# Performance work log

Hardware: AMD Instinct MI355X
Metric: run time of the kernel (lower is better)

## Reference

```python
import jax, jax.numpy as jnp
import numpy as np


def _pred_clampedgrad(x):
    # causal neighbors with zero padding (NCHW)
    n = jnp.pad(x[:, :, :-1, :], ((0, 0), (0, 0), (1, 0), (0, 0)))
    w = jnp.pad(x[:, :, :, :-1], ((0, 0), (0, 0), (0, 0), (1, 0)))
    nw = jnp.pad(x[:, :, :-1, :-1], ((0, 0), (0, 0), (1, 0), (1, 0)))
    pred = jnp.clip(n + w - nw, jnp.minimum(n, w), jnp.maximum(n, w))
    return x - pred


def _calc_entropy_differentiable(x, nbits):
    # Equivalent to the original O(nlevels*N) loop: relu(1-|x-sym|) is exactly
    # linear interpolation onto the two neighboring integer bins, so we build
    # the per-(b,c) soft histogram with one O(N) scatter-add.
    nlevels = 1 << nbits
    xs = (x + 1.0) * ((nlevels - 1) / 2.0)  # map [-1,1] -> [0, nlevels-1]
    B, C, H, W = xs.shape
    flat = xs.reshape(B * C, H * W)
    f = jnp.floor(flat)
    frac = flat - f
    i0 = f.astype(jnp.int32)
    bc = jnp.arange(B * C)[:, None]
    hist = jnp.zeros((B * C, nlevels), xs.dtype)
    hist = hist.at[bc, i0].add(1.0 - frac, mode='drop')  # OOB bins contribute 0 (relu clamp)
    hist = hist.at[bc, i0 + 1].add(frac, mode='drop')
    prob = hist / (H * W)
    safe = jnp.where(prob > 0, prob, 1.0)  # nan_to_num(-0*log2(0)) -> 0
    term = -prob * jnp.log2(safe)
    entropy = jnp.sum(term, axis=1)  # [B*C]
    return jnp.mean(entropy) / nbits


def setup_inputs() -> dict:
    key = jax.random.key(0)
    x = jax.random.uniform(key, (32, 3, 512, 512), jnp.float32, -1.0, 1.0)
    params = jnp.array([-1.0, 0.0, 0.5, 0.0, 0.0, -1.0,
                        0.0, 0.0, 0.0, 0.5, 0.0, 0.0], jnp.float32)
    return {"x": x, "params": params}


def reference(x, params):
    p = params
    r0, g0, b0 = x[:, 0:1], x[:, 1:2], x[:, 2:3]
    r1 = r0 + (p[0] * g0 + p[1] * b0)
    g1 = g0 + (p[2] * r1 + p[3] * b0)
    b1 = b0 + (p[4] * r1 + p[5] * g1)
    r2 = r1 + (p[6] * g1 + p[7] * b1)
    g2 = g1 + (p[8] * r2 + p[9] * b1)
    b2 = b1 + (p[10] * r2 + p[11] * g2)
    y = jnp.concatenate((r2, g2, b2), axis=1)
    y = jnp.fmod(y + 1.0, 2.0) - 1.0  # fmod keeps sign of dividend, same as torch.fmod
    res = _pred_clampedgrad(y)
    return _calc_entropy_differentiable(res, 8)
```

## Files before the change

### kernel.cpp

```cpp
#include <hip/hip_runtime.h>

#define IMG_H 512
#define IMG_W 512
#define RPB 8
#define NROW (RPB + 1)
#define NLEV 256
#define NB 32
#define NC 3
#define NYB (IMG_H / RPB)
#define BINS (NC * NLEV)
#define NBLK (NB * NYB)
#define NTHR 256
#define NWAVE (NTHR / 64)

__device__ uint2    g_pk[NBLK * BINS];
__device__ unsigned g_dropQ[NBLK * NC];
__device__ float    g_ent[NB * NC];
__device__ unsigned g_done = 0;

__device__ __forceinline__ float wrap1(float v) {
    float a = v + 1.0f;
    return a - 2.0f * truncf(0.5f * a) - 1.0f;
}

__device__ __forceinline__ void xform(float& r, float& g, float& bl,
                                      const float* __restrict__ p) {
    float r1 = r + (p[0] * g + p[1] * bl);
    float g1 = g + (p[2] * r1 + p[3] * bl);
    float b1 = bl + (p[4] * r1 + p[5] * g1);
    float r2 = r1 + (p[6] * g1 + p[7] * b1);
    float g2 = g1 + (p[8] * r2 + p[9] * b1);
    float b2 = b1 + (p[10] * r2 + p[11] * g2);
    r = wrap1(r2); g = wrap1(g2); bl = wrap1(b2);
}

__device__ __forceinline__ void accum(float y, float n, float w, float nw,
                                      unsigned* __restrict__ h,
                                      unsigned* __restrict__ drop) {
    float lo = fminf(n, w), hi = fmaxf(n, w);
    float pred = fminf(fmaxf(n + w - nw, lo), hi);
    float xs = (y - pred + 1.0f) * 127.5f;
    float f = floorf(xs);
    float frac = xs - f;
    int i0 = (int)f;
    unsigned fq = (unsigned)(frac * 1024.0f + 0.5f);
    int j0 = (i0 < 0) ? i0 + NLEV : i0;
    if ((unsigned)j0 < (unsigned)NLEV) {
        atomicAdd(&h[j0], (1u << 21) | fq);
        if (i0 == NLEV - 1) atomicAdd(drop, fq);
    }
}

__global__ __launch_bounds__(NTHR) void hist_kernel(const float* __restrict__ x,
                                                    const float* __restrict__ params) {
    __shared__ unsigned lhw[NWAVE][NC][NLEV];
    __shared__ float bnd[NWAVE][NROW][NC];
    __shared__ unsigned dropw[NC];
    const int tid = threadIdx.x;
    const int b = blockIdx.x;
    const int yb = blockIdx.y;
    const int r0 = yb * RPB;
    const int wv = tid >> 6;
    const int lane = tid & 63;

    unsigned* lp = &lhw[0][0][0];
#pragma unroll
    for (int i = tid; i < NWAVE * BINS; i += NTHR) lp[i] = 0u;
    if (tid < NC) dropw[tid] = 0u;

    float p[12];
#pragma unroll
    for (int i = 0; i < 12; ++i) p[i] = params[i];

    const int hw = IMG_H * IMG_W;
    const float2* base = (const float2*)(x + (size_t)(b * 3) * hw) + tid;

    float a0[NROW], a1[NROW], c0[NROW], c1[NROW], e0[NROW], e1[NROW];
#pragma unroll
    for (int rr = 0; rr < NROW; ++rr) {
        if (rr > 0 || r0 > 0) {
            int ro = (r0 - 1 + rr) * (IMG_W / 2);
            float2 vr = base[ro];
            float2 vg = base[ro + hw / 2];
            float2 vb = base[ro + hw];
            a0[rr] = vr.x; a1[rr] = vr.y;
            c0[rr] = vg.x; c1[rr] = vg.y;
            e0[rr] = vb.x; e1[rr] = vb.y;
        } else {
            a0[rr] = a1[rr] = c0[rr] = c1[rr] = e0[rr] = e1[rr] = 0.0f;
        }
    }

#pragma unroll
    for (int rr = 0; rr < NROW; ++rr) {
        xform(a0[rr], c0[rr], e0[rr], p);
        xform(a1[rr], c1[rr], e1[rr], p);
    }

    if (lane == 63) {
#pragma unroll
        for (int rr = 0; rr < NROW; ++rr) {
            bnd[wv][rr][0] = a1[rr];
            bnd[wv][rr][1] = c1[rr];
            bnd[wv][rr][2] = e1[rr];
        }
    }
    __syncthreads();

    const int pw = (wv > 0) ? wv - 1 : 0;
    const float* pwb = &bnd[pw][0][0];
    float bv = pwb[lane < NROW * NC ? lane : 0];
    const bool lz = (lane == 0);

#define RDL(rr, ch) __int_as_float(__builtin_amdgcn_readlane(__float_as_int(bv), (rr) * NC + (ch)))

    unsigned* h0 = &lhw[wv][0][0];
    unsigned* h1 = &lhw[wv][1][0];
    unsigned* h2 = &lhw[wv][2][0];

    float nA0 = a0[0], nA1 = a1[0];
    float nC0 = c0[0], nC1 = c1[0];
    float nE0 = e0[0], nE1 = e1[0];
    float nwA = __shfl_up(a1[0], 1);
    float nwC = __shfl_up(c1[0], 1);
    float nwE = __shfl_up(e1[0], 1);
    {
        float bA = (wv > 0) ? RDL(0, 0) : 0.0f;
        float bC = (wv > 0) ? RDL(0, 1) : 0.0f;
        float bE = (wv > 0) ? RDL(0, 2) : 0.0f;
        if (lz) { nwA = bA; nwC = bC; nwE = bE; }
    }

#pragma unroll
    for (int rr = 1; rr < NROW; ++rr) {
        float uA0 = a0[rr], uA1 = a1[rr];
        float uC0 = c0[rr], uC1 = c1[rr];
        float uE0 = e0[rr], uE1 = e1[rr];
        float vA = __shfl_up(uA1, 1);
        float vC = __shfl_up(uC1, 1);
        float vE = __shfl_up(uE1, 1);
        float bA = (wv > 0) ? RDL(rr, 0) : 0.0f;
        float bC = (wv > 0) ? RDL(rr, 1) : 0.0f;
        float bE = (wv > 0) ? RDL(rr, 2) : 0.0f;
        if (lz) { vA = bA; vC = bC; vE = bE; }
        accum(uA0, nA0, vA, nwA, h0, &dropw[0]);
        accum(uA1, nA1, uA0, nA0, h0, &dropw[0]);
        accum(uC0, nC0, vC, nwC, h1, &dropw[1]);
        accum(uC1, nC1, uC0, nC0, h1, &dropw[1]);
        accum(uE0, nE0, vE, nwE, h2, &dropw[2]);
        accum(uE1, nE1, uE0, nE0, h2, &dropw[2]);
        nwA = vA; nA0 = uA0; nA1 = uA1;
        nwC = vC; nC0 = uC0; nC1 = uC1;
        nwE = vE; nE0 = uE0; nE1 = uE1;
    }
    __syncthreads();

    const int blk = b * NYB + yb;
    uint2* dp = g_pk + (size_t)blk * BINS;
#pragma unroll
    for (int i = tid; i < BINS; i += NTHR) {
        int c = i >> 8, bin = i & 255;
        unsigned cs = 0, qs = 0;
#pragma unroll
        for (int w2 = 0; w2 < NWAVE; ++w2) {
            unsigned v = lhw[w2][c][bin];
            cs += v >> 21;
            qs += v & 0x1FFFFFu;
        }
        dp[i] = make_uint2(cs, qs);
    }
    if (tid < NC) g_dropQ[blk * NC + tid] = dropw[tid];
}

__global__ __launch_bounds__(256) void ent_kernel(float* __restrict__ out) {
    const int g = blockIdx.x;
    const int b = g / NC, c = g % NC;
    const int t = threadIdx.x;
    const uint2* sp = g_pk + (size_t)b * NYB * BINS + c * NLEV + t;
    unsigned cnt = 0, fq = 0;
#pragma unroll
    for (int y = 0; y < NYB; ++y) {
        uint2 v = sp[(size_t)y * BINS];
        cnt += v.x;
        fq  += v.y;
    }
    __shared__ unsigned fsb[NLEV];
    __shared__ unsigned dsh;
    fsb[t] = fq;
    if (t < 64) {
        unsigned d = g_dropQ[(b * NYB + t) * NC + c];
#pragma unroll
        for (int o = 32; o > 0; o >>= 1) d += __shfl_down(d, o);
        if (t == 0) dsh = d;
    }
    __syncthreads();
    unsigned passq = (t == 0) ? (fsb[NLEV - 1] - dsh) : fsb[t - 1];
    float hist = (float)cnt + ((float)passq - (float)fq) * (1.0f / 1024.0f);
    float pr = hist * (1.0f / (float)(IMG_H * IMG_W));
    float term = (pr > 0.0f) ? -pr * log2f(pr) : 0.0f;
#pragma unroll
    for (int o = 32; o > 0; o >>= 1) term += __shfl_down(term, o);
    __shared__ float red[4];
    if ((t & 63) == 0) red[t >> 6] = term;
    __syncthreads();
    if (t == 0) {
        g_ent[g] = red[0] + red[1] + red[2] + red[3];
        __threadfence();
        unsigned prev = atomicAdd(&g_done, 1u);
        if (prev == NB * NC - 1) {
            __threadfence();
            float s = 0.0f;
            for (int i = 0; i < NB * NC; ++i) s += g_ent[i];
            out[0] = s * (1.0f / (float)(NB * NC) / 8.0f);
            g_done = 0;
        }
    }
}

extern "C" void kernel_launch(void* const* d_in, const int* in_sizes, int n_in,
                              void* d_out, int out_size, void* d_ws, size_t ws_size,
                              hipStream_t stream) {
    const float* x = (const float*)d_in[0];
    const float* params = (const float*)d_in[1];
    float* out = (float*)d_out;

    dim3 grid(NB, NYB);
    hist_kernel<<<grid, NTHR, 0, stream>>>(x, params);
    ent_kernel<<<NB * NC, 256, 0, stream>>>(out);
}
```

Measured before the change: 44.76 us.

## Accumulate per-image histograms with global 64-bit atomics and register drop sums

Each histogram block now adds its packed count/fraction bins straight into a per-(batch,channel) 64-bit global accumulator with atomics, replacing the per-block partial histogram buffer. The entropy kernel reads a single value per bin and zeroes it for the next call, so it no longer reduces 64 partials. Drop counts for the top bin are summed in registers, reduced across the wave with shuffles, and committed with one shared atomic per wave instead of a shared atomic per hit. The cost is contention on global atomics (64 blocks per image hit the same 768 bins), plus a reliance on the accumulators starting at zero on the first launch.

```diff
diff --git a/kernel.cpp b/kernel.cpp
--- a/kernel.cpp
+++ b/kernel.cpp
@@ -13,8 +13,8 @@
 #define NTHR 256
 #define NWAVE (NTHR / 64)
 
-__device__ uint2    g_pk[NBLK * BINS];
-__device__ unsigned g_dropQ[NBLK * NC];
+__device__ unsigned long long g_acc[NB * NC * NLEV];
+__device__ unsigned g_dropA[NB * NC];
 __device__ float    g_ent[NB * NC];
 __device__ unsigned g_done = 0;
 
@@ -36,7 +36,7 @@
 
 __device__ __forceinline__ void accum(float y, float n, float w, float nw,
                                       unsigned* __restrict__ h,
-                                      unsigned* __restrict__ drop) {
+                                      unsigned& drop) {
     float lo = fminf(n, w), hi = fmaxf(n, w);
     float pred = fminf(fmaxf(n + w - nw, lo), hi);
     float xs = (y - pred + 1.0f) * 127.5f;
@@ -47,8 +47,8 @@
     int j0 = (i0 < 0) ? i0 + NLEV : i0;
     if ((unsigned)j0 < (unsigned)NLEV) {
         atomicAdd(&h[j0], (1u << 21) | fq);
-        if (i0 == NLEV - 1) atomicAdd(drop, fq);
-    }
+    }
+    drop += (i0 == NLEV - 1) ? fq : 0u;
 }
 
 __global__ __launch_bounds__(NTHR) void hist_kernel(const float* __restrict__ x,
@@ -117,6 +117,7 @@
     unsigned* h0 = &lhw[wv][0][0];
     unsigned* h1 = &lhw[wv][1][0];
     unsigned* h2 = &lhw[wv][2][0];
+    unsigned dr0 = 0u, dr1 = 0u, dr2 = 0u;
 
     float nA0 = a0[0], nA1 = a1[0];
     float nC0 = c0[0], nC1 = c1[0];
@@ -143,20 +144,31 @@
         float bC = (wv > 0) ? RDL(rr, 1) : 0.0f;
         float bE = (wv > 0) ? RDL(rr, 2) : 0.0f;
         if (lz) { vA = bA; vC = bC; vE = bE; }
-        accum(uA0, nA0, vA, nwA, h0, &dropw[0]);
-        accum(uA1, nA1, uA0, nA0, h0, &dropw[0]);
-        accum(uC0, nC0, vC, nwC, h1, &dropw[1]);
-        accum(uC1, nC1, uC0, nC0, h1, &dropw[1]);
-        accum(uE0, nE0, vE, nwE, h2, &dropw[2]);
-        accum(uE1, nE1, uE0, nE0, h2, &dropw[2]);
+        accum(uA0, nA0, vA, nwA, h0, dr0);
+        accum(uA1, nA1, uA0, nA0, h0, dr0);
+        accum(uC0, nC0, vC, nwC, h1, dr1);
+        accum(uC1, nC1, uC0, nC0, h1, dr1);
+        accum(uE0, nE0, vE, nwE, h2, dr2);
+        accum(uE1, nE1, uE0, nE0, h2, dr2);
         nwA = vA; nA0 = uA0; nA1 = uA1;
         nwC = vC; nC0 = uC0; nC1 = uC1;
         nwE = vE; nE0 = uE0; nE1 = uE1;
     }
-    __syncthreads();
-
-    const int blk = b * NYB + yb;
-    uint2* dp = g_pk + (size_t)blk * BINS;
+
+#pragma unroll
+    for (int o = 32; o > 0; o >>= 1) {
+        dr0 += __shfl_down(dr0, o);
+        dr1 += __shfl_down(dr1, o);
+        dr2 += __shfl_down(dr2, o);
+    }
+    if (lz) {
+        atomicAdd(&dropw[0], dr0);
+        atomicAdd(&dropw[1], dr1);
+        atomicAdd(&dropw[2], dr2);
+    }
+    __syncthreads();
+
+    const int gb = b * NC;
 #pragma unroll
     for (int i = tid; i < BINS; i += NTHR) {
         int c = i >> 8, bin = i & 255;
@@ -167,32 +179,23 @@
             cs += v >> 21;
             qs += v & 0x1FFFFFu;
         }
-        dp[i] = make_uint2(cs, qs);
-    }
-    if (tid < NC) g_dropQ[blk * NC + tid] = dropw[tid];
+        atomicAdd(&g_acc[(gb + c) * NLEV + bin],
+                  ((unsigned long long)cs << 32) | (unsigned long long)qs);
+    }
+    if (tid < NC) atomicAdd(&g_dropA[gb + tid], dropw[tid]);
 }
 
 __global__ __launch_bounds__(256) void ent_kernel(float* __restrict__ out) {
     const int g = blockIdx.x;
-    const int b = g / NC, c = g % NC;
     const int t = threadIdx.x;
-    const uint2* sp = g_pk + (size_t)b * NYB * BINS + c * NLEV + t;
-    unsigned cnt = 0, fq = 0;
-#pragma unroll
-    for (int y = 0; y < NYB; ++y) {
-        uint2 v = sp[(size_t)y * BINS];
-        cnt += v.x;
-        fq  += v.y;
-    }
+    unsigned long long v = g_acc[(size_t)g * NLEV + t];
+    g_acc[(size_t)g * NLEV + t] = 0ull;
+    unsigned cnt = (unsigned)(v >> 32);
+    unsigned fq  = (unsigned)(v & 0xFFFFFFFFull);
     __shared__ unsigned fsb[NLEV];
     __shared__ unsigned dsh;
     fsb[t] = fq;
-    if (t < 64) {
-        unsigned d = g_dropQ[(b * NYB + t) * NC + c];
-#pragma unroll
-        for (int o = 32; o > 0; o >>= 1) d += __shfl_down(d, o);
-        if (t == 0) dsh = d;
-    }
+    if (t == 0) { dsh = g_dropA[g]; g_dropA[g] = 0u; }
     __syncthreads();
     unsigned passq = (t == 0) ? (fsb[NLEV - 1] - dsh) : fsb[t - 1];
     float hist = (float)cnt + ((float)passq - (float)fq) * (1.0f / 1024.0f);
```

After: 41.11 us. 1.09x faster.
